# Optimization experiments

Measured on AMD Instinct MI355X. Metric: run time of the kernel, lower is better.

The kernel has to match this reference:

```python
import jax, jax.numpy as jnp
import numpy as np

THRESHOLD = 0.5
NEG_POS_RATIO = 3
VARIANCE = (0.1, 0.2)


def point_form(p):
    # center-form (cx,cy,w,h) -> corner-form (xmin,ymin,xmax,ymax)
    return jnp.concatenate([p[:, :2] - p[:, 2:] / 2, p[:, :2] + p[:, 2:] / 2], axis=-1)


def jaccard(a, b):
    # a: [N,4] corner boxes, b: [P,4] corner boxes -> IoU [N,P]
    lt = jnp.maximum(a[:, None, :2], b[None, :, :2])
    rb = jnp.minimum(a[:, None, 2:], b[None, :, 2:])
    wh = jnp.clip(rb - lt, 0.0)
    inter = wh[..., 0] * wh[..., 1]
    area_a = ((a[:, 2] - a[:, 0]) * (a[:, 3] - a[:, 1]))[:, None]
    area_b = ((b[:, 2] - b[:, 0]) * (b[:, 3] - b[:, 1]))[None, :]
    return inter / (area_a + area_b - inter)


def encode(matched, priors_cf):
    # matched: [P,4] corner GT boxes, priors_cf: [P,4] center-form priors
    g_cxcy = (matched[:, :2] + matched[:, 2:]) / 2 - priors_cf[:, :2]
    g_cxcy = g_cxcy / (VARIANCE[0] * priors_cf[:, 2:])
    g_wh = jnp.log((matched[:, 2:] - matched[:, :2]) / priors_cf[:, 2:]) / VARIANCE[1]
    return jnp.concatenate([g_cxcy, g_wh], axis=-1)  # [P,4]


def match_one(truths, labels, priors_cf):
    # truths: [N,4], labels: [N], priors_cf: [P,4]
    n_obj = truths.shape[0]
    overlaps = jaccard(truths, point_form(priors_cf))          # [N,P]
    best_prior_idx = jnp.argmax(overlaps, axis=1)              # [N] best prior per GT
    best_truth_overlap = jnp.max(overlaps, axis=0)             # [P]
    best_truth_idx = jnp.argmax(overlaps, axis=0)              # [P] best GT per prior
    # ensure every GT keeps its best prior
    best_truth_overlap = best_truth_overlap.at[best_prior_idx].set(2.0)
    best_truth_idx = best_truth_idx.at[best_prior_idx].set(jnp.arange(n_obj))
    matched = truths[best_truth_idx]                           # [P,4]
    conf = jnp.where(best_truth_overlap < THRESHOLD, 0, labels[best_truth_idx] + 1)
    return encode(matched, priors_cf), conf.astype(jnp.int32)


def setup_inputs() -> dict:
    key = jax.random.key(0)
    k1, k2, k3, k4, k5, k6, k7 = jax.random.split(key, 7)
    B, P, C, NOBJ = 64, 24564, 21, 32
    loc_data = jax.random.normal(k1, (B, P, 4), jnp.float32)
    conf_data = jax.random.normal(k2, (B, P, C), jnp.float32)
    p_cxcy = jax.random.uniform(k3, (P, 2), jnp.float32, 0.05, 0.95)
    p_wh = jax.random.uniform(k4, (P, 2), jnp.float32, 0.02, 0.4)
    priors = jnp.concatenate([p_cxcy, p_wh], axis=-1)          # center-form
    t_cxcy = jax.random.uniform(k5, (B, NOBJ, 2), jnp.float32, 0.2, 0.8)
    t_wh = jax.random.uniform(k6, (B, NOBJ, 2), jnp.float32, 0.05, 0.3)
    targets_boxes = jnp.concatenate([t_cxcy - t_wh / 2, t_cxcy + t_wh / 2], axis=-1)
    targets_labels = jax.random.randint(k7, (B, NOBJ), 0, C - 1)  # 0..19, +1 in match
    return {
        "loc_data": loc_data,
        "conf_data": conf_data,
        "priors": priors,
        "targets_boxes": targets_boxes,
        "targets_labels": targets_labels,
    }


def reference(loc_data, conf_data, priors, targets_boxes, targets_labels):
    B, P, C = conf_data.shape
    # targets/priors are detached in the original (.data)
    loc_t, conf_t = jax.vmap(match_one, in_axes=(0, 0, None))(
        jax.lax.stop_gradient(targets_boxes), targets_labels,
        jax.lax.stop_gradient(priors))                          # [B,P,4], [B,P]

    pos = conf_t > 0                                            # [B,P]
    num_pos = jnp.sum(pos, axis=1)                              # [B]

    # localization: smooth L1 on positives, summed
    diff = loc_data - loc_t
    ad = jnp.abs(diff)
    sl1 = jnp.where(ad < 1.0, 0.5 * diff * diff, ad - 0.5)      # [B,P,4]
    loss_l = jnp.sum(sl1 * pos[..., None].astype(sl1.dtype))

    # confidence cross-entropy per prior: lse(x) - x[target]
    lse = jax.nn.logsumexp(conf_data, axis=-1)                  # [B,P]
    gathered = jnp.take_along_axis(conf_data, conf_t[..., None], axis=-1)[..., 0]
    ce_all = lse - gathered                                     # [B,P]

    # hard negative mining: rank negatives by loss, keep top 3*num_pos
    loss_mine = jnp.where(pos, 0.0, ce_all)
    order = jnp.argsort(-loss_mine, axis=1)
    idx_rank = jnp.argsort(order, axis=1)                       # rank of each prior
    num_neg = jnp.clip(NEG_POS_RATIO * num_pos, 0, P - 1)       # [B]
    neg = idx_rank < num_neg[:, None]

    mask = jnp.logical_or(pos, neg)
    loss_c = jnp.sum(ce_all * mask.astype(ce_all.dtype))

    N = jnp.maximum(jnp.sum(num_pos), 1).astype(loss_l.dtype)
    return jnp.stack([loss_l / N, loss_c / N])
```

## Files before the change

### kernel.cpp

```cpp
#include <hip/hip_runtime.h>
#include <stdint.h>

#define THRESH 0.5f
#define VAR0 0.1f
#define VAR1 0.2f

__global__ __launch_bounds__(256) void match_a_kernel(
    const float* __restrict__ priors, const float* __restrict__ tboxes,
    float* __restrict__ best_ov, int* __restrict__ best_idx,
    unsigned long long* __restrict__ part_best,
    int P, int NOBJ, int NBLK)
{
#pragma clang fp contract(off)
    __shared__ float4 tr[64];
    __shared__ float siou[16 * 257];
    __shared__ unsigned long long sp[32][17];
    const int b = blockIdx.y;
    const int bx = blockIdx.x;
    const int tid = threadIdx.x;
    const int p = bx * 256 + tid;
    if (tid < NOBJ) tr[tid] = ((const float4*)tboxes)[(size_t)b * NOBJ + tid];
    __syncthreads();

    const bool valid = (p < P);
    float ax = 0.f, ay = 0.f, bxx = 0.f, byy = 0.f, area_p = 0.f;
    if (valid) {
        float4 pr = ((const float4*)priors)[p];
        ax = pr.x - pr.z * 0.5f;
        ay = pr.y - pr.w * 0.5f;
        bxx = pr.x + pr.z * 0.5f;
        byy = pr.y + pr.w * 0.5f;
        area_p = (bxx - ax) * (byy - ay);
    }

    float bestv = -1.0f;
    int bestn = 0;
    for (int n0 = 0; n0 < NOBJ; n0 += 16) {
        const int jmax = min(16, NOBJ - n0);
        for (int j = 0; j < jmax; ++j) {
            float4 t = tr[n0 + j];
            float iou = -1.0f;
            if (valid) {
                float ltx = fmaxf(t.x, ax), lty = fmaxf(t.y, ay);
                float rbx = fminf(t.z, bxx), rby = fminf(t.w, byy);
                float w = rbx - ltx; if (w < 0.f) w = 0.f;
                float h = rby - lty; if (h < 0.f) h = 0.f;
                float inter = w * h;
                float area_t = (t.z - t.x) * (t.w - t.y);
                iou = inter / ((area_t + area_p) - inter);
                if (iou > bestv) { bestv = iou; bestn = n0 + j; }
            }
            siou[j * 257 + tid] = iou;
        }
        __syncthreads();
        {
            const int n2 = tid & 15, c = tid >> 4;
            if (n2 < jmax) {
                float bv = -1.0f;
                int bs = 0;
                const int base = n2 * 257 + c * 16;
                for (int j2 = 0; j2 < 16; ++j2) {
                    float v = siou[base + j2];
                    if (v > bv) { bv = v; bs = c * 16 + j2; }
                }
                unsigned long long pk = 0ULL;
                if (bv >= 0.f) {
                    unsigned int pp = (unsigned int)(bx * 256 + bs);
                    pk = (((unsigned long long)__float_as_uint(bv)) << 32) |
                         (unsigned long long)(0xFFFFFFFFu - pp);
                }
                sp[n0 + n2][c] = pk;
            }
        }
        __syncthreads();
    }
    if (tid < NOBJ) {
        unsigned long long best = 0ULL;
        for (int c = 0; c < 16; ++c) {
            unsigned long long v = sp[tid][c];
            if (v > best) best = v;
        }
        part_best[((size_t)b * NBLK + bx) * NOBJ + tid] = best;
    }
    if (valid) {
        size_t g = (size_t)b * P + p;
        best_ov[g] = bestv;
        best_idx[g] = bestn;
    }
}

__global__ __launch_bounds__(64) void matchb_fixup_kernel(
    const unsigned long long* __restrict__ part_best,
    float* __restrict__ best_ov, int* __restrict__ best_idx,
    int P, int NOBJ, int NBLK)
{
    const int b = blockIdx.x;
    const int tid = threadIdx.x;
    __shared__ unsigned long long bb[64];
    if (tid < NOBJ) {
        unsigned long long best = 0ULL;
        const unsigned long long* src = part_best + (size_t)b * NBLK * NOBJ + tid;
        for (int j = 0; j < NBLK; ++j) {
            unsigned long long v = src[(size_t)j * NOBJ];
            if (v > best) best = v;
        }
        bb[tid] = best;
    }
    __syncthreads();
    if (tid == 0) {
        for (int n = 0; n < NOBJ; ++n) {
            unsigned int pidx = 0xFFFFFFFFu - (unsigned int)(bb[n] & 0xFFFFFFFFu);
            best_ov[(size_t)b * P + pidx] = 2.0f;
            best_idx[(size_t)b * P + pidx] = n;
        }
    }
}

__global__ __launch_bounds__(256) void main_kernel(
    const float* __restrict__ loc_data, const float* __restrict__ conf_data,
    const float* __restrict__ priors, const float* __restrict__ tboxes,
    const int* __restrict__ labels,
    const float* __restrict__ best_ov, const int* __restrict__ best_idx,
    float* __restrict__ loss_mine,
    float* __restrict__ ll_part, float* __restrict__ pc_part,
    int* __restrict__ np_part,
    int P, int C, int NOBJ, int NBLK)
{
    extern __shared__ float lds[];
    const int b = blockIdx.y;
    const int bx = blockIdx.x;
    const int p0 = bx * 256;
    const int tid = threadIdx.x;
    const int rows = min(256, P - p0);
    const int nflt = rows * C;
    const float* src = conf_data + ((size_t)b * P + p0) * C;

    if ((((uintptr_t)src) & 15) == 0) {
        const int n4 = nflt >> 2;
        const float4* src4 = (const float4*)src;
        for (int i = tid; i < n4; i += 256) ((float4*)lds)[i] = src4[i];
        for (int i = (n4 << 2) + tid; i < nflt; i += 256) lds[i] = src[i];
    } else {
        for (int i = tid; i < nflt; i += 256) lds[i] = src[i];
    }
    __syncthreads();

    float ll = 0.f, pc = 0.f;
    int np = 0;
    if (tid < rows) {
        const int p = p0 + tid;
        const size_t g = (size_t)b * P + p;
        float ov = best_ov[g];
        int ti = best_idx[g];
        int conf_t = 0;
        if (!(ov < THRESH)) conf_t = labels[b * NOBJ + ti] + 1;

        const float* row = lds + tid * C;
        float m = row[0];
        for (int j = 1; j < C; ++j) m = fmaxf(m, row[j]);
        float s = 0.f;
        for (int j = 0; j < C; ++j) s += expf(row[j] - m);
        float ce = (logf(s) + m) - row[conf_t];

        bool pos = (conf_t > 0);
        loss_mine[g] = pos ? 0.f : ce;
        if (pos) {
            np = 1;
            pc = ce;
            float4 t = ((const float4*)tboxes)[(size_t)b * NOBJ + ti];
            float4 pr = ((const float4*)priors)[p];
            float gcx = ((t.x + t.z) * 0.5f - pr.x) / (VAR0 * pr.z);
            float gcy = ((t.y + t.w) * 0.5f - pr.y) / (VAR0 * pr.w);
            float gw  = logf((t.z - t.x) / pr.z) / VAR1;
            float gh  = logf((t.w - t.y) / pr.w) / VAR1;
            float4 ld = ((const float4*)loc_data)[g];
            float d, a;
            d = ld.x - gcx; a = fabsf(d); ll += (a < 1.f) ? 0.5f * d * d : a - 0.5f;
            d = ld.y - gcy; a = fabsf(d); ll += (a < 1.f) ? 0.5f * d * d : a - 0.5f;
            d = ld.z - gw;  a = fabsf(d); ll += (a < 1.f) ? 0.5f * d * d : a - 0.5f;
            d = ld.w - gh;  a = fabsf(d); ll += (a < 1.f) ? 0.5f * d * d : a - 0.5f;
        }
    }

    for (int off = 32; off; off >>= 1) {
        ll += __shfl_down(ll, off, 64);
        pc += __shfl_down(pc, off, 64);
        np += __shfl_down(np, off, 64);
    }
    __shared__ float sll[4], spc[4];
    __shared__ int snp[4];
    const int lane = tid & 63, wid = tid >> 6;
    if (lane == 0) { sll[wid] = ll; spc[wid] = pc; snp[wid] = np; }
    __syncthreads();
    if (tid == 0) {
        size_t slot = (size_t)b * NBLK + bx;
        ll_part[slot] = sll[0] + sll[1] + sll[2] + sll[3];
        pc_part[slot] = spc[0] + spc[1] + spc[2] + spc[3];
        np_part[slot] = snp[0] + snp[1] + snp[2] + snp[3];
    }
}

#define SEL_MAXV 32
__global__ __launch_bounds__(1024) void select_kernel(
    const float* __restrict__ loss_mine, const int* __restrict__ np_part,
    double* __restrict__ neg, int P, int ratio, int NBLK)
{
    const int b = blockIdx.x;
    const int tid = threadIdx.x;
    const int lane = tid & 63, wid = tid >> 6;

    __shared__ int snp_s;
    __shared__ unsigned int hist[16][257];
    __shared__ unsigned int merged[256];
    __shared__ unsigned int sh_sel, sh_k;

    if (tid == 0) snp_s = 0;
    __syncthreads();
    if (tid < NBLK) atomicAdd(&snp_s, np_part[b * NBLK + tid]);
    __syncthreads();
    int k = ratio * snp_s;
    if (k > P - 1) k = P - 1;
    if (k <= 0) {
        if (tid == 0) neg[b] = 0.0;
        return;
    }

    const float* fvals = loss_mine + (size_t)b * P;
    unsigned int vreg[SEL_MAXV];
#pragma unroll
    for (int j = 0; j < SEL_MAXV; ++j) {
        int i = tid + (j << 10);
        vreg[j] = (i < P) ? __float_as_uint(fvals[i]) : 0u;
    }

    unsigned int prefix = 0, mask = 0;
    unsigned int kk = (unsigned int)k;
    for (int shift = 24; shift >= 0; shift -= 8) {
        for (int t = tid; t < 16 * 257; t += 1024) (&hist[0][0])[t] = 0;
        __syncthreads();
        unsigned int* h = hist[wid];
#pragma unroll
        for (int j = 0; j < SEL_MAXV; ++j) {
            int i = tid + (j << 10);
            unsigned int v = vreg[j];
            if (i < P && (v & mask) == prefix)
                atomicAdd(&h[(v >> shift) & 255u], 1u);
        }
        __syncthreads();
        if (tid < 256) {
            unsigned int s = 0;
            for (int w = 0; w < 16; ++w) s += hist[w][tid];
            merged[tid] = s;
        }
        __syncthreads();
        if (wid == 0) {
            unsigned int h0 = merged[4 * lane], h1 = merged[4 * lane + 1];
            unsigned int h2 = merged[4 * lane + 2], h3 = merged[4 * lane + 3];
            unsigned int s3 = h3, s2 = h2 + s3, s1 = h1 + s2, s0 = h0 + s1;
            unsigned int t = s0;
            unsigned int T = t;
            for (int off = 1; off < 64; off <<= 1) {
                unsigned int o = __shfl_down(T, off, 64);
                if (lane + off < 64) T += o;
            }
            unsigned int A = T - t;
            unsigned int S0 = A + s0, S1 = A + s1, S2 = A + s2, S3 = A + s3, S4 = A;
            if (S0 >= kk && S1 < kk) { sh_sel = 4 * lane + 0; sh_k = kk - S1; }
            if (S1 >= kk && S2 < kk) { sh_sel = 4 * lane + 1; sh_k = kk - S2; }
            if (S2 >= kk && S3 < kk) { sh_sel = 4 * lane + 2; sh_k = kk - S3; }
            if (S3 >= kk && S4 < kk) { sh_sel = 4 * lane + 3; sh_k = kk - S4; }
        }
        __syncthreads();
        prefix |= sh_sel << shift;
        mask |= 0xFFu << shift;
        kk = sh_k;
    }
    const float T = __uint_as_float(prefix);

    double sum = 0.0;
    unsigned int cnt = 0;
#pragma unroll
    for (int j = 0; j < SEL_MAXV; ++j) {
        int i = tid + (j << 10);
        if (i < P) {
            float v = __uint_as_float(vreg[j]);
            if (v > T) { sum += (double)v; cnt++; }
        }
    }
    for (int off = 32; off; off >>= 1) {
        sum += __shfl_down(sum, off, 64);
        cnt += __shfl_down(cnt, off, 64);
    }
    __shared__ double sd[16];
    __shared__ unsigned int sc[16];
    if (lane == 0) { sd[wid] = sum; sc[wid] = cnt; }
    __syncthreads();
    if (tid == 0) {
        double S = 0.0;
        unsigned int Cn = 0;
        for (int w = 0; w < 16; ++w) { S += sd[w]; Cn += sc[w]; }
        neg[b] = S + (double)((unsigned int)k - Cn) * (double)T;
    }
}

__global__ __launch_bounds__(256) void finalize_kernel(
    const float* __restrict__ ll_part, const float* __restrict__ pc_part,
    const int* __restrict__ np_part, const double* __restrict__ neg,
    float* __restrict__ out, int NPART, int B)
{
    const int tid = threadIdx.x;
    double ll = 0.0, pc = 0.0, ng = 0.0;
    long long np = 0;
    for (int i = tid; i < NPART; i += 256) {
        ll += (double)ll_part[i];
        pc += (double)pc_part[i];
        np += (long long)np_part[i];
    }
    for (int i = tid; i < B; i += 256) ng += neg[i];

    for (int off = 32; off; off >>= 1) {
        ll += __shfl_down(ll, off, 64);
        pc += __shfl_down(pc, off, 64);
        ng += __shfl_down(ng, off, 64);
        np += __shfl_down(np, off, 64);
    }
    __shared__ double sll[4], spc[4], sng[4];
    __shared__ long long snp[4];
    const int lane = tid & 63, wid = tid >> 6;
    if (lane == 0) { sll[wid] = ll; spc[wid] = pc; sng[wid] = ng; snp[wid] = np; }
    __syncthreads();
    if (tid == 0) {
        double LL = sll[0] + sll[1] + sll[2] + sll[3];
        double PC = spc[0] + spc[1] + spc[2] + spc[3];
        double NG = sng[0] + sng[1] + sng[2] + sng[3];
        long long NP = snp[0] + snp[1] + snp[2] + snp[3];
        if (NP < 1) NP = 1;
        double N = (double)NP;
        out[0] = (float)(LL / N);
        out[1] = (float)((PC + NG) / N);
    }
}

extern "C" void kernel_launch(void* const* d_in, const int* in_sizes, int n_in,
                              void* d_out, int out_size, void* d_ws, size_t ws_size,
                              hipStream_t stream)
{
    const float* loc_data  = (const float*)d_in[0];
    const float* conf_data = (const float*)d_in[1];
    const float* priors    = (const float*)d_in[2];
    const float* tboxes    = (const float*)d_in[3];
    const int*   tlabels   = (const int*)d_in[4];

    const int P = in_sizes[2] / 4;
    const int B = (int)((long long)in_sizes[0] / ((long long)P * 4));
    const int C = (int)((long long)in_sizes[1] / ((long long)B * P));
    const int NOBJ = in_sizes[4] / B;
    const int NBLK = (P + 255) / 256;

    char* ws = (char*)d_ws;
    size_t off = 0;
    double* neg = (double*)(ws + off);            off += (size_t)B * 8;
    off = (off + 255) & ~(size_t)255;
    float* ll_part = (float*)(ws + off);          off += (size_t)B * NBLK * 4;
    off = (off + 255) & ~(size_t)255;
    float* pc_part = (float*)(ws + off);          off += (size_t)B * NBLK * 4;
    off = (off + 255) & ~(size_t)255;
    int* np_part = (int*)(ws + off);              off += (size_t)B * NBLK * 4;
    off = (off + 255) & ~(size_t)255;
    unsigned long long* part_best = (unsigned long long*)(ws + off);
    off += (size_t)B * NBLK * NOBJ * 8;
    off = (off + 255) & ~(size_t)255;
    float* best_ov = (float*)(ws + off);          off += (size_t)B * P * 4;
    off = (off + 255) & ~(size_t)255;
    int* best_idx = (int*)(ws + off);             off += (size_t)B * P * 4;
    off = (off + 255) & ~(size_t)255;
    float* loss_mine = (float*)(ws + off);

    dim3 grid(NBLK, B);
    match_a_kernel<<<grid, 256, 0, stream>>>(priors, tboxes, best_ov, best_idx,
                                             part_best, P, NOBJ, NBLK);
    matchb_fixup_kernel<<<B, 64, 0, stream>>>(part_best, best_ov, best_idx,
                                              P, NOBJ, NBLK);
    size_t smem = (size_t)256 * C * sizeof(float);
    main_kernel<<<grid, 256, smem, stream>>>(loc_data, conf_data, priors, tboxes,
                                             tlabels, best_ov, best_idx, loss_mine,
                                             ll_part, pc_part, np_part,
                                             P, C, NOBJ, NBLK);
    select_kernel<<<B, 1024, 0, stream>>>(loss_mine, np_part, neg, P, 3, NBLK);
    finalize_kernel<<<1, 256, 0, stream>>>(ll_part, pc_part, np_part, neg,
                                           (float*)d_out, B * NBLK, B);
}
```

Measured before the change: 336.9 us.

## Fuse matching with loss kernel and apply best-prior fixup as deltas in select

Merges the IoU matching kernel with the per-prior confidence and localization loss kernel, so best_ov/best_idx no longer round-trip through global memory. The forced best-prior assignment is applied afterwards in the select kernel as per-batch corrections to the loss sums, positive count and loss_mine, instead of a separate fixup pass before the main loss. The final reduction moves into the last select block via an atomic done counter. This removes two launches and about 2·B·P words of global traffic. In exchange the fused kernel needs more LDS per block, and the correction logic (deduplicating priors, recomputing old versus new targets) is more intricate.

```diff
diff --git a/kernel.cpp b/kernel.cpp
--- a/kernel.cpp
+++ b/kernel.cpp
@@ -4,21 +4,29 @@
 #define THRESH 0.5f
 #define VAR0 0.1f
 #define VAR1 0.2f
-
-__global__ __launch_bounds__(256) void match_a_kernel(
+#define SEL_MAXV 32
+
+__global__ __launch_bounds__(256) void fused_kernel(
+    const float* __restrict__ loc_data, const float* __restrict__ conf_data,
     const float* __restrict__ priors, const float* __restrict__ tboxes,
-    float* __restrict__ best_ov, int* __restrict__ best_idx,
+    const int* __restrict__ labels,
     unsigned long long* __restrict__ part_best,
-    int P, int NOBJ, int NBLK)
+    float* __restrict__ loss_mine,
+    float* __restrict__ ll_part, float* __restrict__ pc_part,
+    int* __restrict__ np_part, unsigned int* __restrict__ done_ctr,
+    int P, int C, int NOBJ, int NBLK)
 {
 #pragma clang fp contract(off)
-    __shared__ float4 tr[64];
-    __shared__ float siou[16 * 257];
-    __shared__ unsigned long long sp[32][17];
-    const int b = blockIdx.y;
-    const int bx = blockIdx.x;
-    const int tid = threadIdx.x;
+    extern __shared__ char smem[];
+    float* siou = (float*)smem;
+    unsigned long long (*sp)[17] =
+        (unsigned long long (*)[17])(smem + 16 * 257 * 4);
+    float* confs = (float*)smem;
+    __shared__ float4 tr[32];
+
+    const int b = blockIdx.y, bx = blockIdx.x, tid = threadIdx.x;
     const int p = bx * 256 + tid;
+    if (b == 0 && bx == 0 && tid == 0) *done_ctr = 0;
     if (tid < NOBJ) tr[tid] = ((const float4*)tboxes)[(size_t)b * NOBJ + tid];
     __syncthreads();
 
@@ -82,80 +90,29 @@
         }
         part_best[((size_t)b * NBLK + bx) * NOBJ + tid] = best;
     }
-    if (valid) {
-        size_t g = (size_t)b * P + p;
-        best_ov[g] = bestv;
-        best_idx[g] = bestn;
-    }
-}
-
-__global__ __launch_bounds__(64) void matchb_fixup_kernel(
-    const unsigned long long* __restrict__ part_best,
-    float* __restrict__ best_ov, int* __restrict__ best_idx,
-    int P, int NOBJ, int NBLK)
-{
-    const int b = blockIdx.x;
-    const int tid = threadIdx.x;
-    __shared__ unsigned long long bb[64];
-    if (tid < NOBJ) {
-        unsigned long long best = 0ULL;
-        const unsigned long long* src = part_best + (size_t)b * NBLK * NOBJ + tid;
-        for (int j = 0; j < NBLK; ++j) {
-            unsigned long long v = src[(size_t)j * NOBJ];
-            if (v > best) best = v;
-        }
-        bb[tid] = best;
-    }
-    __syncthreads();
-    if (tid == 0) {
-        for (int n = 0; n < NOBJ; ++n) {
-            unsigned int pidx = 0xFFFFFFFFu - (unsigned int)(bb[n] & 0xFFFFFFFFu);
-            best_ov[(size_t)b * P + pidx] = 2.0f;
-            best_idx[(size_t)b * P + pidx] = n;
-        }
-    }
-}
-
-__global__ __launch_bounds__(256) void main_kernel(
-    const float* __restrict__ loc_data, const float* __restrict__ conf_data,
-    const float* __restrict__ priors, const float* __restrict__ tboxes,
-    const int* __restrict__ labels,
-    const float* __restrict__ best_ov, const int* __restrict__ best_idx,
-    float* __restrict__ loss_mine,
-    float* __restrict__ ll_part, float* __restrict__ pc_part,
-    int* __restrict__ np_part,
-    int P, int C, int NOBJ, int NBLK)
-{
-    extern __shared__ float lds[];
-    const int b = blockIdx.y;
-    const int bx = blockIdx.x;
+    __syncthreads();
+
     const int p0 = bx * 256;
-    const int tid = threadIdx.x;
     const int rows = min(256, P - p0);
     const int nflt = rows * C;
     const float* src = conf_data + ((size_t)b * P + p0) * C;
-
     if ((((uintptr_t)src) & 15) == 0) {
         const int n4 = nflt >> 2;
         const float4* src4 = (const float4*)src;
-        for (int i = tid; i < n4; i += 256) ((float4*)lds)[i] = src4[i];
-        for (int i = (n4 << 2) + tid; i < nflt; i += 256) lds[i] = src[i];
+        for (int i = tid; i < n4; i += 256) ((float4*)confs)[i] = src4[i];
+        for (int i = (n4 << 2) + tid; i < nflt; i += 256) confs[i] = src[i];
     } else {
-        for (int i = tid; i < nflt; i += 256) lds[i] = src[i];
+        for (int i = tid; i < nflt; i += 256) confs[i] = src[i];
     }
     __syncthreads();
 
     float ll = 0.f, pc = 0.f;
     int np = 0;
     if (tid < rows) {
-        const int p = p0 + tid;
         const size_t g = (size_t)b * P + p;
-        float ov = best_ov[g];
-        int ti = best_idx[g];
-        int conf_t = 0;
-        if (!(ov < THRESH)) conf_t = labels[b * NOBJ + ti] + 1;
-
-        const float* row = lds + tid * C;
+        int conf_t = (bestv < THRESH) ? 0 : labels[b * NOBJ + bestn] + 1;
+
+        const float* row = confs + tid * C;
         float m = row[0];
         for (int j = 1; j < C; ++j) m = fmaxf(m, row[j]);
         float s = 0.f;
@@ -167,7 +124,7 @@
         if (pos) {
             np = 1;
             pc = ce;
-            float4 t = ((const float4*)tboxes)[(size_t)b * NOBJ + ti];
+            float4 t = tr[bestn];
             float4 pr = ((const float4*)priors)[p];
             float gcx = ((t.x + t.z) * 0.5f - pr.x) / (VAR0 * pr.z);
             float gcy = ((t.y + t.w) * 0.5f - pr.y) / (VAR0 * pr.w);
@@ -200,144 +157,280 @@
     }
 }
 
-#define SEL_MAXV 32
-__global__ __launch_bounds__(1024) void select_kernel(
-    const float* __restrict__ loss_mine, const int* __restrict__ np_part,
-    double* __restrict__ neg, int P, int ratio, int NBLK)
+__global__ __launch_bounds__(1024) void selectcf_kernel(
+    const float* __restrict__ loc_data, const float* __restrict__ conf_data,
+    const float* __restrict__ priors, const float* __restrict__ tboxes,
+    const int* __restrict__ labels,
+    const unsigned long long* __restrict__ part_best,
+    float* __restrict__ loss_mine,
+    const float* __restrict__ ll_part, const float* __restrict__ pc_part,
+    const int* __restrict__ np_part,
+    double* __restrict__ neg, double* __restrict__ dll_b,
+    double* __restrict__ dpc_b, int* __restrict__ npos_b,
+    unsigned int* __restrict__ done_ctr, float* __restrict__ out,
+    int P, int C, int NOBJ, int NBLK, int B, int ratio)
 {
+#pragma clang fp contract(off)
     const int b = blockIdx.x;
     const int tid = threadIdx.x;
     const int lane = tid & 63, wid = tid >> 6;
 
-    __shared__ int snp_s;
+    __shared__ float4 tr[32];
+    __shared__ unsigned long long sp2[32][17];
+    __shared__ unsigned long long bb[32];
+    __shared__ int2 centry[32];
+    __shared__ double sdll[32], sdpc[32];
+    __shared__ int cnt_s, snp_s, snp_corr;
     __shared__ unsigned int hist[16][257];
     __shared__ unsigned int merged[256];
     __shared__ unsigned int sh_sel, sh_k;
-
-    if (tid == 0) snp_s = 0;
-    __syncthreads();
+    __shared__ double sd[16];
+    __shared__ unsigned int sc[16];
+    __shared__ double negv_s;
+    __shared__ int is_last_s;
+
+    if (tid == 0) { cnt_s = 0; snp_s = 0; snp_corr = 0; negv_s = 0.0; }
+    if (tid < NOBJ) tr[tid] = ((const float4*)tboxes)[(size_t)b * NOBJ + tid];
+    __syncthreads();
+
     if (tid < NBLK) atomicAdd(&snp_s, np_part[b * NBLK + tid]);
-    __syncthreads();
-    int k = ratio * snp_s;
+
+    {
+        const int n = tid & 31, c = tid >> 5;
+        if (tid < 512 && n < NOBJ) {
+            unsigned long long best = 0ULL;
+            for (int j = c; j < NBLK; j += 16) {
+                unsigned long long v = part_best[((size_t)b * NBLK + j) * NOBJ + n];
+                if (v > best) best = v;
+            }
+            sp2[n][c] = best;
+        }
+    }
+    __syncthreads();
+    if (tid < NOBJ) {
+        unsigned long long best = 0ULL;
+        for (int c = 0; c < 16; ++c) {
+            unsigned long long v = sp2[tid][c];
+            if (v > best) best = v;
+        }
+        bb[tid] = best;
+    }
+    __syncthreads();
+
+    if (tid == 0) {
+        int cnt = 0;
+        for (int n = 0; n < NOBJ; ++n) {
+            int pidx = (int)(0xFFFFFFFFu - (unsigned int)(bb[n] & 0xFFFFFFFFu));
+            int f = -1;
+            for (int j = 0; j < cnt; ++j)
+                if (centry[j].x == pidx) f = j;
+            if (f >= 0) centry[f].y = n;
+            else { centry[cnt].x = pidx; centry[cnt].y = n; ++cnt; }
+        }
+        cnt_s = cnt;
+    }
+    __syncthreads();
+
+    if (tid < cnt_s) {
+        const int pidx = centry[tid].x;
+        const int n = centry[tid].y;
+        float4 pr = ((const float4*)priors)[pidx];
+        float ax = pr.x - pr.z * 0.5f;
+        float ay = pr.y - pr.w * 0.5f;
+        float bxx = pr.x + pr.z * 0.5f;
+        float byy = pr.y + pr.w * 0.5f;
+        float area_p = (bxx - ax) * (byy - ay);
+        float bestv = -1.0f;
+        int bestn = 0;
+        for (int nn = 0; nn < NOBJ; ++nn) {
+            float4 t = tr[nn];
+            float ltx = fmaxf(t.x, ax), lty = fmaxf(t.y, ay);
+            float rbx = fminf(t.z, bxx), rby = fminf(t.w, byy);
+            float w = rbx - ltx; if (w < 0.f) w = 0.f;
+            float h = rby - lty; if (h < 0.f) h = 0.f;
+            float inter = w * h;
+            float area_t = (t.z - t.x) * (t.w - t.y);
+            float iou = inter / ((area_t + area_p) - inter);
+            if (iou > bestv) { bestv = iou; bestn = nn; }
+        }
+        const float* row = conf_data + ((size_t)b * P + pidx) * C;
+        float m = row[0];
+        for (int j = 1; j < C; ++j) m = fmaxf(m, row[j]);
+        float s = 0.f;
+        for (int j = 0; j < C; ++j) s += expf(row[j] - m);
+        float lse = logf(s) + m;
+
+        int old_conf = (bestv < THRESH) ? 0 : labels[b * NOBJ + bestn] + 1;
+        int new_conf = labels[b * NOBJ + n] + 1;
+        bool old_pos = (old_conf > 0);
+
+        double dpc = old_pos ? ((double)row[old_conf] - (double)row[new_conf])
+                             : (double)(lse - row[new_conf]);
+
+        const size_t g = (size_t)b * P + pidx;
+        float4 ld = ((const float4*)loc_data)[g];
+        float sl1_new, sl1_old = 0.f;
+        {
+            float4 t = tr[n];
+            float gcx = ((t.x + t.z) * 0.5f - pr.x) / (VAR0 * pr.z);
+            float gcy = ((t.y + t.w) * 0.5f - pr.y) / (VAR0 * pr.w);
+            float gw  = logf((t.z - t.x) / pr.z) / VAR1;
+            float gh  = logf((t.w - t.y) / pr.w) / VAR1;
+            float ll = 0.f, d, a;
+            d = ld.x - gcx; a = fabsf(d); ll += (a < 1.f) ? 0.5f * d * d : a - 0.5f;
+            d = ld.y - gcy; a = fabsf(d); ll += (a < 1.f) ? 0.5f * d * d : a - 0.5f;
+            d = ld.z - gw;  a = fabsf(d); ll += (a < 1.f) ? 0.5f * d * d : a - 0.5f;
+            d = ld.w - gh;  a = fabsf(d); ll += (a < 1.f) ? 0.5f * d * d : a - 0.5f;
+            sl1_new = ll;
+        }
+        if (old_pos) {
+            float4 t = tr[bestn];
+            float gcx = ((t.x + t.z) * 0.5f - pr.x) / (VAR0 * pr.z);
+            float gcy = ((t.y + t.w) * 0.5f - pr.y) / (VAR0 * pr.w);
+            float gw  = logf((t.z - t.x) / pr.z) / VAR1;
+            float gh  = logf((t.w - t.y) / pr.w) / VAR1;
+            float ll = 0.f, d, a;
+            d = ld.x - gcx; a = fabsf(d); ll += (a < 1.f) ? 0.5f * d * d : a - 0.5f;
+            d = ld.y - gcy; a = fabsf(d); ll += (a < 1.f) ? 0.5f * d * d : a - 0.5f;
+            d = ld.z - gw;  a = fabsf(d); ll += (a < 1.f) ? 0.5f * d * d : a - 0.5f;
+            d = ld.w - gh;  a = fabsf(d); ll += (a < 1.f) ? 0.5f * d * d : a - 0.5f;
+            sl1_old = ll;
+        }
+        sdll[tid] = (double)sl1_new - (double)sl1_old;
+        sdpc[tid] = dpc;
+        if (!old_pos) {
+            atomicAdd(&snp_corr, 1);
+            loss_mine[g] = 0.f;
+        }
+    }
+    __syncthreads();
+
+    int k = ratio * (snp_s + snp_corr);
     if (k > P - 1) k = P - 1;
-    if (k <= 0) {
-        if (tid == 0) neg[b] = 0.0;
-        return;
-    }
-
-    const float* fvals = loss_mine + (size_t)b * P;
-    unsigned int vreg[SEL_MAXV];
-#pragma unroll
-    for (int j = 0; j < SEL_MAXV; ++j) {
-        int i = tid + (j << 10);
-        vreg[j] = (i < P) ? __float_as_uint(fvals[i]) : 0u;
-    }
-
-    unsigned int prefix = 0, mask = 0;
-    unsigned int kk = (unsigned int)k;
-    for (int shift = 24; shift >= 0; shift -= 8) {
-        for (int t = tid; t < 16 * 257; t += 1024) (&hist[0][0])[t] = 0;
-        __syncthreads();
-        unsigned int* h = hist[wid];
+
+    if (k > 0) {
+        const float* fvals = loss_mine + (size_t)b * P;
+        unsigned int vreg[SEL_MAXV];
 #pragma unroll
         for (int j = 0; j < SEL_MAXV; ++j) {
             int i = tid + (j << 10);
-            unsigned int v = vreg[j];
-            if (i < P && (v & mask) == prefix)
-                atomicAdd(&h[(v >> shift) & 255u], 1u);
-        }
+            vreg[j] = (i < P) ? __float_as_uint(fvals[i]) : 0u;
+        }
+        unsigned int prefix = 0, mask = 0;
+        unsigned int kk = (unsigned int)k;
+        for (int shift = 24; shift >= 0; shift -= 8) {
+            for (int t = tid; t < 16 * 257; t += 1024) (&hist[0][0])[t] = 0;
+            __syncthreads();
+            unsigned int* h = hist[wid];
+#pragma unroll
+            for (int j = 0; j < SEL_MAXV; ++j) {
+                int i = tid + (j << 10);
+                unsigned int v = vreg[j];
+                if (i < P && (v & mask) == prefix)
+                    atomicAdd(&h[(v >> shift) & 255u], 1u);
+            }
+            __syncthreads();
+            if (tid < 256) {
+                unsigned int s = 0;
+                for (int w = 0; w < 16; ++w) s += hist[w][tid];
+                merged[tid] = s;
+            }
+            __syncthreads();
+            if (wid == 0) {
+                unsigned int h0 = merged[4 * lane], h1 = merged[4 * lane + 1];
+                unsigned int h2 = merged[4 * lane + 2], h3 = merged[4 * lane + 3];
+                unsigned int s3 = h3, s2 = h2 + s3, s1 = h1 + s2, s0 = h0 + s1;
+                unsigned int t = s0;
+                unsigned int T = t;
+                for (int off = 1; off < 64; off <<= 1) {
+                    unsigned int o = __shfl_down(T, off, 64);
+                    if (lane + off < 64) T += o;
+                }
+                unsigned int A = T - t;
+                unsigned int S0 = A + s0, S1 = A + s1, S2 = A + s2, S3 = A + s3, S4 = A;
+                if (S0 >= kk && S1 < kk) { sh_sel = 4 * lane + 0; sh_k = kk - S1; }
+                if (S1 >= kk && S2 < kk) { sh_sel = 4 * lane + 1; sh_k = kk - S2; }
+                if (S2 >= kk && S3 < kk) { sh_sel = 4 * lane + 2; sh_k = kk - S3; }
+                if (S3 >= kk && S4 < kk) { sh_sel = 4 * lane + 3; sh_k = kk - S4; }
+            }
+            __syncthreads();
+            prefix |= sh_sel << shift;
+            mask |= 0xFFu << shift;
+            kk = sh_k;
+        }
+        const float T = __uint_as_float(prefix);
+
+        double sum = 0.0;
+        unsigned int cnt = 0;
+#pragma unroll
+        for (int j = 0; j < SEL_MAXV; ++j) {
+            int i = tid + (j << 10);
+            if (i < P) {
+                float v = __uint_as_float(vreg[j]);
+                if (v > T) { sum += (double)v; cnt++; }
+            }
+        }
+        for (int off = 32; off; off >>= 1) {
+            sum += __shfl_down(sum, off, 64);
+            cnt += __shfl_down(cnt, off, 64);
+        }
+        if (lane == 0) { sd[wid] = sum; sc[wid] = cnt; }
         __syncthreads();
-        if (tid < 256) {
-            unsigned int s = 0;
-            for (int w = 0; w < 16; ++w) s += hist[w][tid];
-            merged[tid] = s;
-        }
-        __syncthreads();
-        if (wid == 0) {
-            unsigned int h0 = merged[4 * lane], h1 = merged[4 * lane + 1];
-            unsigned int h2 = merged[4 * lane + 2], h3 = merged[4 * lane + 3];
-            unsigned int s3 = h3, s2 = h2 + s3, s1 = h1 + s2, s0 = h0 + s1;
-            unsigned int t = s0;
-            unsigned int T = t;
-            for (int off = 1; off < 64; off <<= 1) {
-                unsigned int o = __shfl_down(T, off, 64);
-                if (lane + off < 64) T += o;
-            }
-            unsigned int A = T - t;
-            unsigned int S0 = A + s0, S1 = A + s1, S2 = A + s2, S3 = A + s3, S4 = A;
-            if (S0 >= kk && S1 < kk) { sh_sel = 4 * lane + 0; sh_k = kk - S1; }
-            if (S1 >= kk && S2 < kk) { sh_sel = 4 * lane + 1; sh_k = kk - S2; }
-            if (S2 >= kk && S3 < kk) { sh_sel = 4 * lane + 2; sh_k = kk - S3; }
-            if (S3 >= kk && S4 < kk) { sh_sel = 4 * lane + 3; sh_k = kk - S4; }
-        }
-        __syncthreads();
-        prefix |= sh_sel << shift;
-        mask |= 0xFFu << shift;
-        kk = sh_k;
-    }
-    const float T = __uint_as_float(prefix);
-
-    double sum = 0.0;
-    unsigned int cnt = 0;
-#pragma unroll
-    for (int j = 0; j < SEL_MAXV; ++j) {
-        int i = tid + (j << 10);
-        if (i < P) {
-            float v = __uint_as_float(vreg[j]);
-            if (v > T) { sum += (double)v; cnt++; }
-        }
+        if (tid == 0) {
+            double S = 0.0;
+            unsigned int Cn = 0;
+            for (int w = 0; w < 16; ++w) { S += sd[w]; Cn += sc[w]; }
+            negv_s = S + (double)((unsigned int)k - Cn) * (double)T;
+        }
+    }
+    __syncthreads();
+
+    if (tid == 0) {
+        double DL = 0.0, DP = 0.0;
+        for (int j = 0; j < cnt_s; ++j) { DL += sdll[j]; DP += sdpc[j]; }
+        neg[b] = negv_s;
+        dll_b[b] = DL;
+        dpc_b[b] = DP;
+        npos_b[b] = snp_s + snp_corr;
+        __threadfence();
+        unsigned int old = atomicAdd(done_ctr, 1u);
+        is_last_s = (old == (unsigned int)B - 1) ? 1 : 0;
+    }
+    __syncthreads();
+    if (!is_last_s) return;
+    __threadfence();
+
+    double LL = 0.0, PC = 0.0, NG = 0.0;
+    long long NP = 0;
+    const int NPART = B * NBLK;
+    for (int i = tid; i < NPART; i += 1024) {
+        LL += (double)ll_part[i];
+        PC += (double)pc_part[i];
+    }
+    for (int i = tid; i < B; i += 1024) {
+        NG += neg[i];
+        LL += dll_b[i];
+        PC += dpc_b[i];
+        NP += (long long)npos_b[i];
     }
     for (int off = 32; off; off >>= 1) {
-        sum += __shfl_down(sum, off, 64);
-        cnt += __shfl_down(cnt, off, 64);
-    }
-    __shared__ double sd[16];
-    __shared__ unsigned int sc[16];
-    if (lane == 0) { sd[wid] = sum; sc[wid] = cnt; }
+        LL += __shfl_down(LL, off, 64);
+        PC += __shfl_down(PC, off, 64);
+        NG += __shfl_down(NG, off, 64);
+        NP += __shfl_down(NP, off, 64);
+    }
+    __shared__ double fll[16], fpc[16], fng[16];
+    __shared__ long long fnp[16];
+    if (lane == 0) { fll[wid] = LL; fpc[wid] = PC; fng[wid] = NG; fnp[wid] = NP; }
     __syncthreads();
     if (tid == 0) {
-        double S = 0.0;
-        unsigned int Cn = 0;
-        for (int w = 0; w < 16; ++w) { S += sd[w]; Cn += sc[w]; }
-        neg[b] = S + (double)((unsigned int)k - Cn) * (double)T;
-    }
-}
-
-__global__ __launch_bounds__(256) void finalize_kernel(
-    const float* __restrict__ ll_part, const float* __restrict__ pc_part,
-    const int* __restrict__ np_part, const double* __restrict__ neg,
-    float* __restrict__ out, int NPART, int B)
-{
-    const int tid = threadIdx.x;
-    double ll = 0.0, pc = 0.0, ng = 0.0;
-    long long np = 0;
-    for (int i = tid; i < NPART; i += 256) {
-        ll += (double)ll_part[i];
-        pc += (double)pc_part[i];
-        np += (long long)np_part[i];
-    }
-    for (int i = tid; i < B; i += 256) ng += neg[i];
-
-    for (int off = 32; off; off >>= 1) {
-        ll += __shfl_down(ll, off, 64);
-        pc += __shfl_down(pc, off, 64);
-        ng += __shfl_down(ng, off, 64);
-        np += __shfl_down(np, off, 64);
-    }
-    __shared__ double sll[4], spc[4], sng[4];
-    __shared__ long long snp[4];
-    const int lane = tid & 63, wid = tid >> 6;
-    if (lane == 0) { sll[wid] = ll; spc[wid] = pc; sng[wid] = ng; snp[wid] = np; }
-    __syncthreads();
-    if (tid == 0) {
-        double LL = sll[0] + sll[1] + sll[2] + sll[3];
-        double PC = spc[0] + spc[1] + spc[2] + spc[3];
-        double NG = sng[0] + sng[1] + sng[2] + sng[3];
-        long long NP = snp[0] + snp[1] + snp[2] + snp[3];
-        if (NP < 1) NP = 1;
-        double N = (double)NP;
-        out[0] = (float)(LL / N);
-        out[1] = (float)((PC + NG) / N);
+        double L = 0.0, Pc = 0.0, Ng = 0.0;
+        long long Np = 0;
+        for (int w = 0; w < 16; ++w) { L += fll[w]; Pc += fpc[w]; Ng += fng[w]; Np += fnp[w]; }
+        if (Np < 1) Np = 1;
+        double N = (double)Np;
+        out[0] = (float)(L / N);
+        out[1] = (float)((Pc + Ng) / N);
     }
 }
 
@@ -359,34 +452,38 @@
 
     char* ws = (char*)d_ws;
     size_t off = 0;
-    double* neg = (double*)(ws + off);            off += (size_t)B * 8;
-    off = (off + 255) & ~(size_t)255;
-    float* ll_part = (float*)(ws + off);          off += (size_t)B * NBLK * 4;
-    off = (off + 255) & ~(size_t)255;
-    float* pc_part = (float*)(ws + off);          off += (size_t)B * NBLK * 4;
-    off = (off + 255) & ~(size_t)255;
-    int* np_part = (int*)(ws + off);              off += (size_t)B * NBLK * 4;
+    unsigned int* done_ctr = (unsigned int*)(ws + off);  off += 256;
+    double* neg = (double*)(ws + off);                   off += (size_t)B * 8;
+    off = (off + 255) & ~(size_t)255;
+    double* dll_b = (double*)(ws + off);                 off += (size_t)B * 8;
+    off = (off + 255) & ~(size_t)255;
+    double* dpc_b = (double*)(ws + off);                 off += (size_t)B * 8;
+    off = (off + 255) & ~(size_t)255;
+    int* npos_b = (int*)(ws + off);                      off += (size_t)B * 4;
+    off = (off + 255) & ~(size_t)255;
+    float* ll_part = (float*)(ws + off);                 off += (size_t)B * NBLK * 4;
+    off = (off + 255) & ~(size_t)255;
+    float* pc_part = (float*)(ws + off);                 off += (size_t)B * NBLK * 4;
+    off = (off + 255) & ~(size_t)255;
+    int* np_part = (int*)(ws + off);                     off += (size_t)B * NBLK * 4;
     off = (off + 255) & ~(size_t)255;
     unsigned long long* part_best = (unsigned long long*)(ws + off);
     off += (size_t)B * NBLK * NOBJ * 8;
     off = (off + 255) & ~(size_t)255;
-    float* best_ov = (float*)(ws + off);          off += (size_t)B * P * 4;
-    off = (off + 255) & ~(size_t)255;
-    int* best_idx = (int*)(ws + off);             off += (size_t)B * P * 4;
-    off = (off + 255) & ~(size_t)255;
     float* loss_mine = (float*)(ws + off);
 
+    size_t smem_match = 16 * 257 * 4 + 32 * 17 * 8;
+    size_t smem_conf = (size_t)256 * C * 4;
+    size_t smem = smem_match > smem_conf ? smem_match : smem_conf;
+
     dim3 grid(NBLK, B);
-    match_a_kernel<<<grid, 256, 0, stream>>>(priors, tboxes, best_ov, best_idx,
-                                             part_best, P, NOBJ, NBLK);
-    matchb_fixup_kernel<<<B, 64, 0, stream>>>(part_best, best_ov, best_idx,
-                                              P, NOBJ, NBLK);
-    size_t smem = (size_t)256 * C * sizeof(float);
-    main_kernel<<<grid, 256, smem, stream>>>(loc_data, conf_data, priors, tboxes,
-                                             tlabels, best_ov, best_idx, loss_mine,
-                                             ll_part, pc_part, np_part,
-                                             P, C, NOBJ, NBLK);
-    select_kernel<<<B, 1024, 0, stream>>>(loss_mine, np_part, neg, P, 3, NBLK);
-    finalize_kernel<<<1, 256, 0, stream>>>(ll_part, pc_part, np_part, neg,
-                                           (float*)d_out, B * NBLK, B);
+    fused_kernel<<<grid, 256, smem, stream>>>(
+        loc_data, conf_data, priors, tboxes, tlabels,
+        part_best, loss_mine, ll_part, pc_part, np_part, done_ctr,
+        P, C, NOBJ, NBLK);
+    selectcf_kernel<<<B, 1024, 0, stream>>>(
+        loc_data, conf_data, priors, tboxes, tlabels,
+        part_best, loss_mine, ll_part, pc_part, np_part,
+        neg, dll_b, dpc_b, npos_b, done_ctr, (float*)d_out,
+        P, C, NOBJ, NBLK, B, 3);
 }
```

Result: faster. 308.8 us (-8.3%).
